# Performance work log

Measured on AMD Instinct MI355X. Metric: run time of the kernel, lower is better.

## Reference

```python
import jax, jax.numpy as jnp
import numpy as np

N_DST = 8192   # rows of x (scatter destination)
N_SRC = 32768  # rows of t (scatter source)
H, W = 64, 32  # feature slab per row


def setup_inputs() -> dict:
    key = jax.random.key(0)
    k1, k2, k3 = jax.random.split(key, 3)
    x = jax.random.normal(k1, (N_DST, H, W), dtype=jnp.float32)
    t = jax.random.normal(k2, (N_SRC, H, W), dtype=jnp.float32)
    index = jax.random.randint(k3, (N_SRC,), 0, N_DST, dtype=jnp.int64)
    return {"x": x, "t": t, "index": index}


def reference(x, t, index):
    # torch: x.index_reduce_(-3, index, t, 'amax', include_self=True)
    # Scatter-max of t rows into x along dim 0; include_self=True means the
    # original x values participate in the max, which is exactly scatter-max.
    return x.at[index].max(t)
```

## Files before the change

### kernel.cpp

```cpp
#include <hip/hip_runtime.h>

#define NDST 8192
#define NSRC 32768
#define HW   2048
#define HW4  (HW/4)
#define CAP  64


__global__ void fill_kernel(const int* __restrict__ index,
                            int* __restrict__ counts,
                            int* __restrict__ bucket) {
    int i = blockIdx.x * blockDim.x + threadIdx.x;
    if (i < NSRC) {
        int dst = index[i];
        int pos = atomicAdd(&counts[dst], 1);
        if (pos < CAP) bucket[dst * CAP + pos] = i;
    }
}

__global__ void gather_max_kernel(const float* __restrict__ x,
                                  const float* __restrict__ t,
                                  const int* __restrict__ counts,
                                  const int* __restrict__ bucket,
                                  float* __restrict__ out) {
    const int wave = threadIdx.x >> 6;
    const int lane = threadIdx.x & 63;
    const int dst = blockIdx.x * 4 + wave;

    const int cnt_raw = counts[dst];
    const int cnt = cnt_raw < CAP ? cnt_raw : CAP;
    const int base = dst * CAP;

    const float4* xrow = (const float4*)(x + (size_t)dst * HW);
    float4* orow = (float4*)(out + (size_t)dst * HW);

    float4 acc[8];
    #pragma unroll
    for (int k = 0; k < 8; ++k) acc[k] = xrow[k * 64 + lane];

    int s_next = (cnt > 0) ? bucket[base] : 0;
    for (int j = 0; j < cnt; ++j) {
        const int src = s_next;
        if (j + 1 < cnt) s_next = bucket[base + j + 1];
        const float4* trow = (const float4*)(t + (size_t)src * HW);
        float4 b[8];
        #pragma unroll
        for (int k = 0; k < 8; ++k) b[k] = trow[k * 64 + lane];
        #pragma unroll
        for (int k = 0; k < 8; ++k) {
            acc[k].x = fmaxf(acc[k].x, b[k].x);
            acc[k].y = fmaxf(acc[k].y, b[k].y);
            acc[k].z = fmaxf(acc[k].z, b[k].z);
            acc[k].w = fmaxf(acc[k].w, b[k].w);
        }
    }

    #pragma unroll
    for (int k = 0; k < 8; ++k) orow[k * 64 + lane] = acc[k];
}

extern "C" void kernel_launch(void* const* d_in, const int* in_sizes, int n_in,
                              void* d_out, int out_size, void* d_ws, size_t ws_size,
                              hipStream_t stream) {
    const float* x   = (const float*)d_in[0];
    const float* t   = (const float*)d_in[1];
    const int* index = (const int*)d_in[2];
    float* out = (float*)d_out;

    int* counts = (int*)d_ws;
    int* bucket = counts + NDST;

    hipMemsetAsync(counts, 0, NDST * sizeof(int), stream);
    fill_kernel<<<NSRC / 256, 256, 0, stream>>>(index, counts, bucket);
    gather_max_kernel<<<NDST / 4, 256, 0, stream>>>(x, t, counts, bucket, out);
}
```

Measured before the change: 429.7 us.

## Split each destination row across two waves with nontemporal loads and software prefetch

Each destination row is now handled by two wavefronts, each owning half of the 2048-float slab, which doubles the number of waves and halves per-wave register use. The t-row loads are software-pipelined so the next source row is fetched before the current one is reduced. Loads and stores use nontemporal hints, and launch bounds request higher occupancy. The bucket list and counts are now read twice, once per half-row wave, which adds a small amount of redundant index traffic.

Measured after the change: 402.3 us. 6.4% less time.

```diff
diff --git a/kernel.cpp b/kernel.cpp
--- a/kernel.cpp
+++ b/kernel.cpp
@@ -5,6 +5,8 @@
 #define HW   2048
 #define HW4  (HW/4)
 #define CAP  64
+
+typedef float f4 __attribute__((ext_vector_type(4)));
 
 
 __global__ void fill_kernel(const int* __restrict__ index,
@@ -18,36 +20,58 @@
     }
 }
 
-__global__ void gather_max_kernel(const float* __restrict__ x,
-                                  const float* __restrict__ t,
-                                  const int* __restrict__ counts,
-                                  const int* __restrict__ bucket,
-                                  float* __restrict__ out) {
+__global__ __launch_bounds__(256, 4)
+void gather_max_kernel(const float* __restrict__ x,
+                       const float* __restrict__ t,
+                       const int* __restrict__ counts,
+                       const int* __restrict__ bucket,
+                       float* __restrict__ out) {
     const int wave = threadIdx.x >> 6;
     const int lane = threadIdx.x & 63;
-    const int dst = blockIdx.x * 4 + wave;
+    int slot = blockIdx.x * 4 + wave;
+    slot = __builtin_amdgcn_readfirstlane(slot);
+    const int dst  = slot >> 1;
+    const int half = slot & 1;
 
     const int cnt_raw = counts[dst];
     const int cnt = cnt_raw < CAP ? cnt_raw : CAP;
     const int base = dst * CAP;
 
-    const float4* xrow = (const float4*)(x + (size_t)dst * HW);
-    float4* orow = (float4*)(out + (size_t)dst * HW);
+    const size_t row4 = (size_t)dst * HW4 + half * 256 + lane;
 
-    float4 acc[8];
+    const f4* xp = (const f4*)x + row4;
+    f4 acc[4];
     #pragma unroll
-    for (int k = 0; k < 8; ++k) acc[k] = xrow[k * 64 + lane];
+    for (int k = 0; k < 4; ++k)
+        acc[k] = __builtin_nontemporal_load(xp + k * 64);
 
-    int s_next = (cnt > 0) ? bucket[base] : 0;
-    for (int j = 0; j < cnt; ++j) {
-        const int src = s_next;
-        if (j + 1 < cnt) s_next = bucket[base + j + 1];
-        const float4* trow = (const float4*)(t + (size_t)src * HW);
-        float4 b[8];
+    if (cnt > 0) {
+        int src = bucket[base];
+        const f4* tp = (const f4*)t + ((size_t)src * HW4 + half * 256 + lane);
+        f4 b[4];
         #pragma unroll
-        for (int k = 0; k < 8; ++k) b[k] = trow[k * 64 + lane];
+        for (int k = 0; k < 4; ++k)
+            b[k] = __builtin_nontemporal_load(tp + k * 64);
+
+        for (int j = 1; j < cnt; ++j) {
+            int nsrc = bucket[base + j];
+            const f4* np = (const f4*)t + ((size_t)nsrc * HW4 + half * 256 + lane);
+            f4 nb[4];
+            #pragma unroll
+            for (int k = 0; k < 4; ++k)
+                nb[k] = __builtin_nontemporal_load(np + k * 64);
+            #pragma unroll
+            for (int k = 0; k < 4; ++k) {
+                acc[k].x = fmaxf(acc[k].x, b[k].x);
+                acc[k].y = fmaxf(acc[k].y, b[k].y);
+                acc[k].z = fmaxf(acc[k].z, b[k].z);
+                acc[k].w = fmaxf(acc[k].w, b[k].w);
+            }
+            #pragma unroll
+            for (int k = 0; k < 4; ++k) b[k] = nb[k];
+        }
         #pragma unroll
-        for (int k = 0; k < 8; ++k) {
+        for (int k = 0; k < 4; ++k) {
             acc[k].x = fmaxf(acc[k].x, b[k].x);
             acc[k].y = fmaxf(acc[k].y, b[k].y);
             acc[k].z = fmaxf(acc[k].z, b[k].z);
@@ -55,8 +79,10 @@
         }
     }
 
+    f4* op = (f4*)out + row4;
     #pragma unroll
-    for (int k = 0; k < 8; ++k) orow[k * 64 + lane] = acc[k];
+    for (int k = 0; k < 4; ++k)
+        __builtin_nontemporal_store(acc[k], op + k * 64);
 }
 
 extern "C" void kernel_launch(void* const* d_in, const int* in_sizes, int n_in,
@@ -72,5 +98,5 @@
 
     hipMemsetAsync(counts, 0, NDST * sizeof(int), stream);
     fill_kernel<<<NSRC / 256, 256, 0, stream>>>(index, counts, bucket);
-    gather_max_kernel<<<NDST / 4, 256, 0, stream>>>(x, t, counts, bucket, out);
+    gather_max_kernel<<<(NDST * 2) / 4, 256, 0, stream>>>(x, t, counts, bucket, out);
 }
```
